# Performance work log

Measured on AMD Instinct MI355X. Metric: run time of the kernel, lower is better.

Reference implementation:

```python
import jax, jax.numpy as jnp
import numpy as np

B, S, I, H = 64, 512, 1024, 1024


def setup_inputs() -> dict:
    key = jax.random.key(0)
    ks = jax.random.split(key, 17)
    stdv = 1.0 / np.sqrt(H)
    u = lambda k, shape: jax.random.uniform(k, shape, jnp.float32, -stdv, stdv)
    inp = {
        "inputs": jax.random.normal(ks[0], (B, S, I), jnp.float32),
        "h0": jnp.zeros((B, 1, H), jnp.float32),
        "c0": jnp.zeros((B, 1, H), jnp.float32),
        # gate weights: input->hidden [H, I], hidden->hidden [H, H], biases [H]
        "w_ii": u(ks[1], (H, I)), "w_hi": u(ks[2], (H, H)), "b_ii": u(ks[3], (H,)), "b_hi": u(ks[4], (H,)),
        "w_if": u(ks[5], (H, I)), "w_hf": u(ks[6], (H, H)), "b_if": u(ks[7], (H,)), "b_hf": u(ks[8], (H,)),
        "w_ig": u(ks[9], (H, I)), "w_hg": u(ks[10], (H, H)), "b_ig": u(ks[11], (H,)), "b_hg": u(ks[12], (H,)),
        "w_io": u(ks[13], (H, I)), "w_ho": u(ks[14], (H, H)), "b_io": u(ks[15], (H,)), "b_ho": u(ks[16], (H,)),
    }
    return inp


def reference(inputs, h0, c0,
              w_ii, w_hi, b_ii, b_hi,
              w_if, w_hf, b_if, b_hf,
              w_ig, w_hg, b_ig, b_hg,
              w_io, w_ho, b_io, b_ho):
    # inputs: [B, S, I]; state: h0/c0 [B, 1, H]
    def step(carry, x_t):  # x_t: [B, I]
        h, c = carry  # [B, H] each
        i = jax.nn.sigmoid(x_t @ w_ii.T + b_ii + h @ w_hi.T + b_hi)
        f = jax.nn.sigmoid(x_t @ w_if.T + b_if + h @ w_hf.T + b_hf)
        g = jnp.tanh(x_t @ w_ig.T + b_ig + h @ w_hg.T + b_hg)
        o = jax.nn.sigmoid(x_t @ w_io.T + b_io + h @ w_ho.T + b_ho)
        c_next = f * c + i * g
        h_next = o * jnp.tanh(c_next)
        return (h_next, c_next), h_next

    xs = jnp.swapaxes(inputs, 0, 1)  # [S, B, I]
    (h_f, c_f), hs = jax.lax.scan(step, (h0[:, 0, :], c0[:, 0, :]), xs)
    hidden_seq = jnp.swapaxes(hs, 0, 1)  # [B, S, H]
    return hidden_seq, h_f[:, None, :], c_f[:, None, :]
```

## Files before the change

kernel.cpp:

```cpp
#include <hip/hip_runtime.h>
#include <hip/hip_bf16.h>
#include <hip/hip_cooperative_groups.h>

namespace cg = cooperative_groups;

using s16x8 = __attribute__((ext_vector_type(8))) short;
using f32x4 = __attribute__((ext_vector_type(4))) float;

constexpr int BB = 64;
constexpr int SS = 512;
constexpr int II = 1024;
constexpr int HH = 1024;

__device__ __forceinline__ unsigned short f2bf(float f) {
  unsigned u = __float_as_uint(f);
  unsigned r = u + 0x7fffu + ((u >> 16) & 1u);
  return (unsigned short)(r >> 16);
}
__device__ __forceinline__ float bf2f(unsigned short h) {
  return __uint_as_float(((unsigned)h) << 16);
}

__global__ void __launch_bounds__(256) pack_w_single(
    const float* __restrict__ wii, const float* __restrict__ whi_,
    const float* __restrict__ wif, const float* __restrict__ whf,
    const float* __restrict__ wig, const float* __restrict__ whg,
    const float* __restrict__ wio, const float* __restrict__ who,
    unsigned short* __restrict__ Wpk)
{
  unsigned f = blockIdx.x * 256 + threadIdx.x;
  int lane = f & 63;
  int kb   = (f >> 6) & 31;
  int ks   = (f >> 11) & 1;
  int blk  = (int)(f >> 12);
  int n = lane & 15, u = lane >> 4;
  int hc = blk * 4 + (n >> 2), g = n & 3;
  int k  = kb * 32 + u * 8;
  const float* wi4[4] = {wii, wif, wig, wio};
  const float* wh4[4] = {whi_, whf, whg, who};
  const float* src = (ks == 0) ? (wi4[g] + (size_t)hc * 1024 + k)
                               : (wh4[g] + (size_t)hc * 1024 + k);
  float4 v0 = *(const float4*)src;
  float4 v1 = *(const float4*)(src + 4);
  s16x8 r;
  r[0] = (short)f2bf(v0.x); r[1] = (short)f2bf(v0.y);
  r[2] = (short)f2bf(v0.z); r[3] = (short)f2bf(v0.w);
  r[4] = (short)f2bf(v1.x); r[5] = (short)f2bf(v1.y);
  r[6] = (short)f2bf(v1.z); r[7] = (short)f2bf(v1.w);
  *(s16x8*)(Wpk + (size_t)f * 8) = r;
}

__global__ void __launch_bounds__(256) pack_bias(
    const float* __restrict__ bii, const float* __restrict__ bhi,
    const float* __restrict__ bif, const float* __restrict__ bhf,
    const float* __restrict__ big, const float* __restrict__ bhg,
    const float* __restrict__ bio, const float* __restrict__ bho,
    float* __restrict__ biasC)
{
  int cidx = blockIdx.x * 256 + threadIdx.x;
  int col = cidx & 15, blk = cidx >> 4;
  int hc = blk * 4 + (col >> 2), g = col & 3;
  const float* bi4[4] = {bii, bif, big, bio};
  const float* bh4[4] = {bhi, bhf, bhg, bho};
  biasC[cidx] = bi4[g][hc] + bh4[g][hc];
}

__global__ void __launch_bounds__(256) conv_x(const float* __restrict__ x,
                                              unsigned short* __restrict__ xb)
{
  int bs = blockIdx.x;
  int b = bs >> 9, s = bs & 511;
  float4 v = *(const float4*)(x + ((size_t)b * 512 + s) * 1024 + threadIdx.x * 4);
  *(ushort4*)(xb + ((size_t)s * 64 + b) * 1024 + threadIdx.x * 4) =
      make_ushort4(f2bf(v.x), f2bf(v.y), f2bf(v.z), f2bf(v.w));
}

__global__ void __launch_bounds__(256) conv_out_t(const unsigned short* __restrict__ hseq,
                                                  float* __restrict__ out)
{
  __shared__ float tile[64][257];
  int bid = blockIdx.x;
  int t = bid >> 2, q = bid & 3;
  const unsigned short* src = hseq + (size_t)(t + 1) * 65536 + q * 16384;
#pragma unroll
  for (int it = 0; it < 16; ++it) {
    int idx = it * 256 + threadIdx.x;
    int blkg = idx >> 6;
    int b = idx & 63;
    ushort4 v = *(const ushort4*)(src + idx * 4);
    int c = blkg * 4;
    tile[b][c + 0] = bf2f(v.x); tile[b][c + 1] = bf2f(v.y);
    tile[b][c + 2] = bf2f(v.z); tile[b][c + 3] = bf2f(v.w);
  }
  __syncthreads();
#pragma unroll
  for (int it = 0; it < 16; ++it) {
    int idx = it * 256 + threadIdx.x;
    int b = idx >> 6;
    int c4 = idx & 63;
    float4 o = *(const float4*)&tile[b][c4 * 4];
    *(float4*)(out + ((size_t)b * 512 + t) * 1024 + q * 256 + c4 * 4) = o;
  }
}

__device__ __forceinline__ void hbar_arrive(int* cnt, int blk, int kbar) {
  int g = blk & 7;
  int* lp = cnt + g * 16;
  __hip_atomic_fetch_add(lp, 1, __ATOMIC_RELAXED, __HIP_MEMORY_SCOPE_AGENT);
  if (blk < 8) {
    while (__hip_atomic_load(lp, __ATOMIC_RELAXED, __HIP_MEMORY_SCOPE_AGENT) < 32 * kbar)
      __builtin_amdgcn_s_sleep(1);
    __hip_atomic_fetch_add(cnt + 8 * 16, 1, __ATOMIC_RELAXED, __HIP_MEMORY_SCOPE_AGENT);
  }
}
__device__ __forceinline__ void hbar_spin(int* cnt, int kbar) {
  int* gp = cnt + 8 * 16;
  while (__hip_atomic_load(gp, __ATOMIC_RELAXED, __HIP_MEMORY_SCOPE_AGENT) < 8 * kbar)
    __builtin_amdgcn_s_sleep(1);
}

__device__ __forceinline__ void gemm_q(const unsigned short* __restrict__ aptr,
                                       const s16x8* __restrict__ WlV, int wb,
                                       f32x4& out) {
  s16x8 a[8];
#pragma unroll
  for (int kb = 0; kb < 8; ++kb) a[kb] = *(const s16x8*)(aptr + kb * 32);
  f32x4 c0_ = {0.f, 0.f, 0.f, 0.f}, c1_ = c0_;
#pragma unroll
  for (int kb = 0; kb < 8; kb += 2) {
    c0_ = __builtin_amdgcn_mfma_f32_16x16x32_bf16(a[kb],     WlV[wb + kb * 64],       c0_, 0, 0, 0);
    c1_ = __builtin_amdgcn_mfma_f32_16x16x32_bf16(a[kb + 1], WlV[wb + (kb + 1) * 64], c1_, 0, 0, 0);
  }
  out = c0_ + c1_;
}

__device__ __forceinline__ void gemm_qh(const unsigned short* __restrict__ p0,
                                        const s16x8* __restrict__ WlV, int wb,
                                        f32x4& out) {
  s16x8 a[8];
#pragma unroll
  for (int kb = 0; kb < 8; ++kb) {
    ushort4 lo = *(const ushort4*)(p0 + kb * 2048);
    ushort4 hi = *(const ushort4*)(p0 + kb * 2048 + 256);
    s16x8 v;
    v[0] = (short)lo.x; v[1] = (short)lo.y; v[2] = (short)lo.z; v[3] = (short)lo.w;
    v[4] = (short)hi.x; v[5] = (short)hi.y; v[6] = (short)hi.z; v[7] = (short)hi.w;
    a[kb] = v;
  }
  f32x4 c0_ = {0.f, 0.f, 0.f, 0.f}, c1_ = c0_;
#pragma unroll
  for (int kb = 0; kb < 8; kb += 2) {
    c0_ = __builtin_amdgcn_mfma_f32_16x16x32_bf16(a[kb],     WlV[wb + kb * 64],       c0_, 0, 0, 0);
    c1_ = __builtin_amdgcn_mfma_f32_16x16x32_bf16(a[kb + 1], WlV[wb + (kb + 1) * 64], c1_, 0, 0, 0);
  }
  out = c0_ + c1_;
}

__global__ void __launch_bounds__(1024, 1) lstm_fast13(
    const unsigned short* __restrict__ Wpk,
    const float* __restrict__ biasC,
    const unsigned short* __restrict__ xb,
    unsigned short* __restrict__ hseq,
    int* __restrict__ cnt,
    const float* __restrict__ h0,
    const float* __restrict__ c0,
    float* __restrict__ out)
{
  __shared__ s16x8 WlV[4096];
  __shared__ float gX[4][64][17];
  __shared__ float gH[4][64][17];
  __shared__ float biasLds[16];
  __shared__ short hOutLds[64][4];

  const int tid  = threadIdx.x;
  const int blk  = blockIdx.x;
  const int wave = tid >> 6, lane = tid & 63;
  const int m  = wave & 3;
  const int kq = wave >> 2;
  const int arow = m * 16 + (lane & 15);
  const int u    = lane >> 4;
  const int koff = u * 8;
  const int aoff = arow * 1024 + kq * 256 + koff;
  const int hoff = (kq * 64 + u * 2) * 256 + arow * 4;
  const int wxb = (kq * 8) * 64 + lane;
  const int whb = (32 + kq * 8) * 64 + lane;
  const int drow = m * 16 + u * 4;
  const int dcol = lane & 15;

  {
    const s16x8* src = (const s16x8*)(Wpk + (size_t)blk * 32768);
#pragma unroll
    for (int it = 0; it < 4; ++it) WlV[it * 1024 + tid] = src[it * 1024 + tid];
  }
  if (tid < 16) biasLds[tid] = biasC[blk * 16 + tid];

  if (tid < 64) {
    float4 v = *(const float4*)(h0 + (size_t)tid * 1024 + blk * 4);
    unsigned lo = (unsigned)f2bf(v.x) | ((unsigned)f2bf(v.y) << 16);
    unsigned hi = (unsigned)f2bf(v.z) | ((unsigned)f2bf(v.w) << 16);
    unsigned long long w = (unsigned long long)lo | ((unsigned long long)hi << 32);
    __hip_atomic_store((unsigned long long*)(hseq + blk * 256 + tid * 4),
                       w, __ATOMIC_RELAXED, __HIP_MEMORY_SCOPE_AGENT);
  }
  const int rb_batch = tid >> 2, rb_j = tid & 3;
  float c_reg = 0.f;
  if (tid < 256) c_reg = c0[rb_batch * 1024 + blk * 4 + rb_j];

  __syncthreads();

  f32x4 xacc;
  gemm_q(xb + aoff, WlV, wxb, xacc);

  if (tid == 256) { hbar_arrive(cnt, blk, 1); hbar_spin(cnt, 1); }
  __syncthreads();

  for (int t = 0; t < SS; ++t) {
#pragma unroll
    for (int r = 0; r < 4; ++r) gX[kq][drow + r][dcol] = xacc[r];
    {
      f32x4 hs;
      gemm_qh(hseq + (size_t)t * 65536 + hoff, WlV, whb, hs);
#pragma unroll
      for (int r = 0; r < 4; ++r) gH[kq][drow + r][dcol] = hs[r];
    }
    __syncthreads();

    if (tid < 256) {
      int c0i = rb_j * 4;
      float si = (gX[0][rb_batch][c0i + 0] + gX[1][rb_batch][c0i + 0])
               + (gX[2][rb_batch][c0i + 0] + gX[3][rb_batch][c0i + 0])
               + (gH[0][rb_batch][c0i + 0] + gH[1][rb_batch][c0i + 0])
               + (gH[2][rb_batch][c0i + 0] + gH[3][rb_batch][c0i + 0]) + biasLds[c0i + 0];
      float sf = (gX[0][rb_batch][c0i + 1] + gX[1][rb_batch][c0i + 1])
               + (gX[2][rb_batch][c0i + 1] + gX[3][rb_batch][c0i + 1])
               + (gH[0][rb_batch][c0i + 1] + gH[1][rb_batch][c0i + 1])
               + (gH[2][rb_batch][c0i + 1] + gH[3][rb_batch][c0i + 1]) + biasLds[c0i + 1];
      float sg = (gX[0][rb_batch][c0i + 2] + gX[1][rb_batch][c0i + 2])
               + (gX[2][rb_batch][c0i + 2] + gX[3][rb_batch][c0i + 2])
               + (gH[0][rb_batch][c0i + 2] + gH[1][rb_batch][c0i + 2])
               + (gH[2][rb_batch][c0i + 2] + gH[3][rb_batch][c0i + 2]) + biasLds[c0i + 2];
      float so = (gX[0][rb_batch][c0i + 3] + gX[1][rb_batch][c0i + 3])
               + (gX[2][rb_batch][c0i + 3] + gX[3][rb_batch][c0i + 3])
               + (gH[0][rb_batch][c0i + 3] + gH[1][rb_batch][c0i + 3])
               + (gH[2][rb_batch][c0i + 3] + gH[3][rb_batch][c0i + 3]) + biasLds[c0i + 3];
      float iv = 1.f / (1.f + __expf(-si));
      float fv = 1.f / (1.f + __expf(-sf));
      float gv = tanhf(sg);
      float ov = 1.f / (1.f + __expf(-so));
      c_reg = fv * c_reg + iv * gv;
      float hv = ov * tanhf(c_reg);
      hOutLds[rb_batch][rb_j] = (short)f2bf(hv);
      if (t == SS - 1) {
        int hcg = blk * 4 + rb_j;
        out[(size_t)BB * SS * HH + rb_batch * 1024 + hcg] = hv;
        out[(size_t)BB * SS * HH + 65536 + rb_batch * 1024 + hcg] = c_reg;
      }
    }
    __syncthreads();

    if (tid < 64) {
      unsigned long long v = *(const unsigned long long*)&hOutLds[tid][0];
      __hip_atomic_store(
          (unsigned long long*)(hseq + (size_t)(t + 1) * 65536 + blk * 256 + tid * 4),
          v, __ATOMIC_RELAXED, __HIP_MEMORY_SCOPE_AGENT);
    }
    __syncthreads();

    if (t + 1 < SS) {
      if (tid == 256) hbar_arrive(cnt, blk, t + 2);
      gemm_q(xb + (size_t)(t + 1) * 65536 + aoff, WlV, wxb, xacc);
      if (tid == 256) hbar_spin(cnt, t + 2);
      __syncthreads();
    }
  }
}

__global__ void __launch_bounds__(256) pack_w(
    const float* __restrict__ wii, const float* __restrict__ whi_,
    const float* __restrict__ wif, const float* __restrict__ whf,
    const float* __restrict__ wig, const float* __restrict__ whg,
    const float* __restrict__ wio, const float* __restrict__ who,
    unsigned short* __restrict__ Whi, unsigned short* __restrict__ Wlo)
{
  size_t idx = ((size_t)blockIdx.x * 256 + threadIdx.x) * 4;
  int k   = (int)(idx & 2047);
  int rg  = (int)(idx >> 11);
  int row = rg & 15;
  int blk = rg >> 4;
  int hc  = blk * 4 + (row >> 2);
  int g   = row & 3;
  const float* wi4[4] = {wii, wif, wig, wio};
  const float* wh4[4] = {whi_, whf, whg, who};
  const float* src = (k < 1024) ? (wi4[g] + (size_t)hc * 1024 + k)
                                : (wh4[g] + (size_t)hc * 1024 + (k - 1024));
  float4 v = *(const float4*)src;
  float vv[4] = {v.x, v.y, v.z, v.w};
  unsigned short h_[4], l_[4];
#pragma unroll
  for (int j = 0; j < 4; ++j) {
    unsigned short h = f2bf(vv[j]);
    h_[j] = h;
    l_[j] = f2bf(vv[j] - bf2f(h));
  }
  *(ushort4*)(Whi + idx) = make_ushort4(h_[0], h_[1], h_[2], h_[3]);
  *(ushort4*)(Wlo + idx) = make_ushort4(l_[0], l_[1], l_[2], l_[3]);
}

__global__ void __launch_bounds__(512, 1) lstm_seq_legacy(
    const unsigned short* __restrict__ W,
    const float* __restrict__ biasC,
    const float* __restrict__ xin,
    unsigned short* __restrict__ hb,
    const float* __restrict__ h0,
    const float* __restrict__ c0,
    float* __restrict__ out)
{
  __shared__ short Wl[2][16][2048];
  __shared__ float gLds[2][64][17];
  __shared__ float biasLds[16];

  const int tid  = threadIdx.x;
  const int blk  = blockIdx.x;
  const int wave = tid >> 6;
  const int lane = tid & 63;
  const int m    = wave >> 1;
  const int ks   = wave & 1;
  const int arow = m * 16 + (lane & 15);
  const int koff = (lane >> 4) * 8;
  const int brow = lane & 15;
  const int bswz = (brow & 7) << 4;

  {
    const char* srcH = (const char*)W + (size_t)blk * 65536;
    const char* srcL = (const char*)W + 16777216u + (size_t)blk * 65536;
    char* dstH = (char*)&Wl[0][0][0];
    char* dstL = (char*)&Wl[1][0][0];
#pragma unroll
    for (int it = 0; it < 8; ++it) {
      int boff = it * 8192 + tid * 16;
      int row  = boff >> 12;
      int colb = boff & 4095;
      int dsw  = row * 4096 + (colb ^ ((row & 7) << 4));
      *(int4*)(dstH + dsw) = *(const int4*)(srcH + boff);
      *(int4*)(dstL + dsw) = *(const int4*)(srcL + boff);
    }
  }
  if (tid < 16) biasLds[tid] = biasC[blk * 16 + tid];
  if (tid < 256) {
    int e = blk * 256 + tid;
    hb[e] = f2bf(h0[e]);
  }
  const int rb_batch = tid >> 2, rb_j = tid & 3;
  float c_reg = 0.f;
  if (tid < 256) c_reg = c0[rb_batch * 1024 + blk * 4 + rb_j];

  cg::grid_group grid = cg::this_grid();
  __syncthreads();
  grid.sync();

  const char* wrow = (const char*)&Wl[0][0][0] + brow * 4096;
  const int kbyte = ks * 2048;

  for (int t = 0; t < SS; ++t) {
    const unsigned short* hcur = hb + (t & 1) * 65536;
    f32x4 accH = {0.f, 0.f, 0.f, 0.f};
    f32x4 accL = {0.f, 0.f, 0.f, 0.f};

    if (ks == 1) {
      const unsigned short* aptr = hcur + arow * 1024 + koff;
#pragma unroll
      for (int kk = 0; kk < 1024; kk += 32) {
        s16x8 a = *(const s16x8*)(aptr + kk);
        int cb = (kbyte + (kk + koff) * 2) ^ bswz;
        s16x8 bh = *(const s16x8*)(wrow + cb);
        s16x8 bl = *(const s16x8*)(wrow + 65536 + cb);
        accH = __builtin_amdgcn_mfma_f32_16x16x32_bf16(a, bh, accH, 0, 0, 0);
        accL = __builtin_amdgcn_mfma_f32_16x16x32_bf16(a, bl, accL, 0, 0, 0);
      }
    } else {
      const float* xp = xin + ((size_t)arow * 512 + t) * 1024 + koff;
#pragma unroll
      for (int kk = 0; kk < 1024; kk += 32) {
        float4 f0 = *(const float4*)(xp + kk);
        float4 f1 = *(const float4*)(xp + kk + 4);
        s16x8 a;
        a[0] = (short)f2bf(f0.x); a[1] = (short)f2bf(f0.y);
        a[2] = (short)f2bf(f0.z); a[3] = (short)f2bf(f0.w);
        a[4] = (short)f2bf(f1.x); a[5] = (short)f2bf(f1.y);
        a[6] = (short)f2bf(f1.z); a[7] = (short)f2bf(f1.w);
        int cb = ((kk + koff) * 2) ^ bswz;
        s16x8 bh = *(const s16x8*)(wrow + cb);
        s16x8 bl = *(const s16x8*)(wrow + 65536 + cb);
        accH = __builtin_amdgcn_mfma_f32_16x16x32_bf16(a, bh, accH, 0, 0, 0);
        accL = __builtin_amdgcn_mfma_f32_16x16x32_bf16(a, bl, accL, 0, 0, 0);
      }
    }

    {
      f32x4 acc = accH + accL;
      int drow = m * 16 + (lane >> 4) * 4;
      int dcol = lane & 15;
#pragma unroll
      for (int r = 0; r < 4; ++r) gLds[ks][drow + r][dcol] = acc[r];
    }
    __syncthreads();

    if (tid < 256) {
      int c0i = rb_j * 4;
      float si = gLds[0][rb_batch][c0i + 0] + gLds[1][rb_batch][c0i + 0] + biasLds[c0i + 0];
      float sf = gLds[0][rb_batch][c0i + 1] + gLds[1][rb_batch][c0i + 1] + biasLds[c0i + 1];
      float sg = gLds[0][rb_batch][c0i + 2] + gLds[1][rb_batch][c0i + 2] + biasLds[c0i + 2];
      float so = gLds[0][rb_batch][c0i + 3] + gLds[1][rb_batch][c0i + 3] + biasLds[c0i + 3];
      float iv = 1.f / (1.f + __expf(-si));
      float fv = 1.f / (1.f + __expf(-sf));
      float gv = tanhf(sg);
      float ov = 1.f / (1.f + __expf(-so));
      c_reg = fv * c_reg + iv * gv;
      float hv = ov * tanhf(c_reg);
      int hcg = blk * 4 + rb_j;
      out[(size_t)rb_batch * (SS * HH) + (size_t)t * HH + hcg] = hv;
      hb[((t + 1) & 1) * 65536 + rb_batch * 1024 + hcg] = f2bf(hv);
      if (t == SS - 1) {
        out[(size_t)BB * SS * HH + rb_batch * 1024 + hcg] = hv;
        out[(size_t)BB * SS * HH + 65536 + rb_batch * 1024 + hcg] = c_reg;
      }
    }
    grid.sync();
  }
}

extern "C" void kernel_launch(void* const* d_in, const int* in_sizes, int n_in,
                              void* d_out, int out_size, void* d_ws, size_t ws_size,
                              hipStream_t stream) {
  const float* xin = (const float*)d_in[0];
  const float* h0  = (const float*)d_in[1];
  const float* c0  = (const float*)d_in[2];
  const float* wii = (const float*)d_in[3];
  const float* whi = (const float*)d_in[4];
  const float* bii = (const float*)d_in[5];
  const float* bhi = (const float*)d_in[6];
  const float* wif = (const float*)d_in[7];
  const float* whf = (const float*)d_in[8];
  const float* bif = (const float*)d_in[9];
  const float* bhf = (const float*)d_in[10];
  const float* wig = (const float*)d_in[11];
  const float* whg = (const float*)d_in[12];
  const float* big = (const float*)d_in[13];
  const float* bhg = (const float*)d_in[14];
  const float* wio = (const float*)d_in[15];
  const float* who = (const float*)d_in[16];
  const float* bio = (const float*)d_in[17];
  const float* bho = (const float*)d_in[18];
  float* out = (float*)d_out;

  char* ws = (char*)d_ws;
  unsigned short* Wpk   = (unsigned short*)ws;
  float*          biasC = (float*)(ws + 33554432);
  int*            cnt   = (int*)(ws + 33570816);
  unsigned short* hseq  = (unsigned short*)(ws + 33636352);
  unsigned short* xb    = (unsigned short*)(ws + 100876288);
  const size_t need_fast_xb = 100876288ull + 67108864ull;

  unsigned short* Wl_  = (unsigned short*)ws;
  unsigned short* hb   = (unsigned short*)(ws + 33570816);

  if (ws_size >= need_fast_xb) {
    pack_w_single<<<4096, 256, 0, stream>>>(wii, whi, wif, whf, wig, whg, wio, who, Wpk);
    pack_bias<<<16, 256, 0, stream>>>(bii, bhi, bif, bhf, big, bhg, bio, bho, biasC);
    conv_x<<<32768, 256, 0, stream>>>(xin, xb);
    hipMemsetAsync(cnt, 0, 4096, stream);

    void* ka[] = {(void*)&Wpk, (void*)&biasC, (void*)&xb,
                  (void*)&hseq, (void*)&cnt, (void*)&h0, (void*)&c0, (void*)&out};
    hipLaunchCooperativeKernel(reinterpret_cast<const void*>(&lstm_fast13),
                               dim3(256), dim3(1024), ka, 0, stream);
    conv_out_t<<<2048, 256, 0, stream>>>(hseq, out);
  } else {
    pack_w<<<8192, 256, 0, stream>>>(wii, whi, wif, whf, wig, whg, wio, who,
                                     Wl_, Wl_ + 8388608);
    pack_bias<<<16, 256, 0, stream>>>(bii, bhi, bif, bhf, big, bhg, bio, bho, biasC);
    void* ka[] = {(void*)&Wl_, (void*)&biasC, (void*)&xin,
                  (void*)&hb, (void*)&h0, (void*)&c0, (void*)&out};
    hipLaunchCooperativeKernel(reinterpret_cast<const void*>(&lstm_seq_legacy),
                               dim3(256), dim3(512), ka, 0, stream);
  }
}
```

Before: 3.438 ms.

## Publish h via wave shuffles and overlap next-step x GEMM with gate math

The gate-computing threads now pack their bf16 h outputs with cross-lane shuffles and store them straight to global memory. This drops the LDS staging buffer and one block-wide barrier per timestep. Waves 4-15, which sit idle during the gate math, start the next step's input-projection GEMM in that window, so only waves 0-3 run it after the barrier. Bias values move from LDS into registers. The x-GEMM is now split across waves around the barrier, which lengthens the critical path for the h store only slightly but depends on the shuffle lanes lining up with rb_j.

Result: slower. 4.017 ms (+16.9%).

```diff
diff --git a/kernel.cpp b/kernel.cpp
--- a/kernel.cpp
+++ b/kernel.cpp
@@ -156,7 +156,7 @@
   out = c0_ + c1_;
 }
 
-__global__ void __launch_bounds__(1024, 1) lstm_fast13(
+__global__ void __launch_bounds__(1024, 1) lstm_fast14(
     const unsigned short* __restrict__ Wpk,
     const float* __restrict__ biasC,
     const unsigned short* __restrict__ xb,
@@ -170,7 +170,6 @@
   __shared__ float gX[4][64][17];
   __shared__ float gH[4][64][17];
   __shared__ float biasLds[16];
-  __shared__ short hOutLds[64][4];
 
   const int tid  = threadIdx.x;
   const int blk  = blockIdx.x;
@@ -203,8 +202,12 @@
                        w, __ATOMIC_RELAXED, __HIP_MEMORY_SCOPE_AGENT);
   }
   const int rb_batch = tid >> 2, rb_j = tid & 3;
-  float c_reg = 0.f;
-  if (tid < 256) c_reg = c0[rb_batch * 1024 + blk * 4 + rb_j];
+  float c_reg = 0.f, b0 = 0.f, b1 = 0.f, b2 = 0.f, b3 = 0.f;
+  if (tid < 256) {
+    const float* bp = biasC + blk * 16 + rb_j * 4;
+    b0 = bp[0]; b1 = bp[1]; b2 = bp[2]; b3 = bp[3];
+    c_reg = c0[rb_batch * 1024 + blk * 4 + rb_j];
+  }
 
   __syncthreads();
 
@@ -230,45 +233,48 @@
       float si = (gX[0][rb_batch][c0i + 0] + gX[1][rb_batch][c0i + 0])
                + (gX[2][rb_batch][c0i + 0] + gX[3][rb_batch][c0i + 0])
                + (gH[0][rb_batch][c0i + 0] + gH[1][rb_batch][c0i + 0])
-               + (gH[2][rb_batch][c0i + 0] + gH[3][rb_batch][c0i + 0]) + biasLds[c0i + 0];
+               + (gH[2][rb_batch][c0i + 0] + gH[3][rb_batch][c0i + 0]) + b0;
       float sf = (gX[0][rb_batch][c0i + 1] + gX[1][rb_batch][c0i + 1])
                + (gX[2][rb_batch][c0i + 1] + gX[3][rb_batch][c0i + 1])
                + (gH[0][rb_batch][c0i + 1] + gH[1][rb_batch][c0i + 1])
-               + (gH[2][rb_batch][c0i + 1] + gH[3][rb_batch][c0i + 1]) + biasLds[c0i + 1];
+               + (gH[2][rb_batch][c0i + 1] + gH[3][rb_batch][c0i + 1]) + b1;
       float sg = (gX[0][rb_batch][c0i + 2] + gX[1][rb_batch][c0i + 2])
                + (gX[2][rb_batch][c0i + 2] + gX[3][rb_batch][c0i + 2])
                + (gH[0][rb_batch][c0i + 2] + gH[1][rb_batch][c0i + 2])
-               + (gH[2][rb_batch][c0i + 2] + gH[3][rb_batch][c0i + 2]) + biasLds[c0i + 2];
+               + (gH[2][rb_batch][c0i + 2] + gH[3][rb_batch][c0i + 2]) + b2;
       float so = (gX[0][rb_batch][c0i + 3] + gX[1][rb_batch][c0i + 3])
                + (gX[2][rb_batch][c0i + 3] + gX[3][rb_batch][c0i + 3])
                + (gH[0][rb_batch][c0i + 3] + gH[1][rb_batch][c0i + 3])
-               + (gH[2][rb_batch][c0i + 3] + gH[3][rb_batch][c0i + 3]) + biasLds[c0i + 3];
+               + (gH[2][rb_batch][c0i + 3] + gH[3][rb_batch][c0i + 3]) + b3;
       float iv = 1.f / (1.f + __expf(-si));
       float fv = 1.f / (1.f + __expf(-sf));
       float gv = tanhf(sg);
       float ov = 1.f / (1.f + __expf(-so));
       c_reg = fv * c_reg + iv * gv;
       float hv = ov * tanhf(c_reg);
-      hOutLds[rb_batch][rb_j] = (short)f2bf(hv);
+      unsigned short me16 = f2bf(hv);
+      unsigned v01 = (unsigned)me16 |
+                     ((((unsigned)__shfl_xor((int)(unsigned)me16, 1)) & 0xffffu) << 16);
+      unsigned v23 = (unsigned)__shfl_xor((int)v01, 2);
+      if (rb_j == 0) {
+        unsigned long long w = (unsigned long long)v01 | ((unsigned long long)v23 << 32);
+        __hip_atomic_store(
+            (unsigned long long*)(hseq + (size_t)(t + 1) * 65536 + blk * 256 + rb_batch * 4),
+            w, __ATOMIC_RELAXED, __HIP_MEMORY_SCOPE_AGENT);
+      }
       if (t == SS - 1) {
         int hcg = blk * 4 + rb_j;
         out[(size_t)BB * SS * HH + rb_batch * 1024 + hcg] = hv;
         out[(size_t)BB * SS * HH + 65536 + rb_batch * 1024 + hcg] = c_reg;
       }
-    }
-    __syncthreads();
-
-    if (tid < 64) {
-      unsigned long long v = *(const unsigned long long*)&hOutLds[tid][0];
-      __hip_atomic_store(
-          (unsigned long long*)(hseq + (size_t)(t + 1) * 65536 + blk * 256 + tid * 4),
-          v, __ATOMIC_RELAXED, __HIP_MEMORY_SCOPE_AGENT);
+    } else if (t + 1 < SS) {
+      gemm_q(xb + (size_t)(t + 1) * 65536 + aoff, WlV, wxb, xacc);
     }
     __syncthreads();
 
     if (t + 1 < SS) {
       if (tid == 256) hbar_arrive(cnt, blk, t + 2);
-      gemm_q(xb + (size_t)(t + 1) * 65536 + aoff, WlV, wxb, xacc);
+      if (wave < 4) gemm_q(xb + (size_t)(t + 1) * 65536 + aoff, WlV, wxb, xacc);
       if (tid == 256) hbar_spin(cnt, t + 2);
       __syncthreads();
     }
@@ -472,7 +478,7 @@
 
     void* ka[] = {(void*)&Wpk, (void*)&biasC, (void*)&xb,
                   (void*)&hseq, (void*)&cnt, (void*)&h0, (void*)&c0, (void*)&out};
-    hipLaunchCooperativeKernel(reinterpret_cast<const void*>(&lstm_fast13),
+    hipLaunchCooperativeKernel(reinterpret_cast<const void*>(&lstm_fast14),
                                dim3(256), dim3(1024), ka, 0, stream);
     conv_out_t<<<2048, 256, 0, stream>>>(hseq, out);
   } else {
```
